# Performance work log

Measured on AMD Instinct MI355X. Metric: run time of the kernel, lower is better.

The kernel has to match this reference:

```python
import jax, jax.numpy as jnp
import numpy as np

B, V, C = 256, 50, 40
VOCAB, D, H, NH, T = 10000, 256, 256, 8, 1000


def setup_inputs():
    key = jax.random.key(0)
    ks = jax.random.split(key, 24)
    f = lambda k, shape, s=0.05: jax.random.normal(k, shape, jnp.float32) * s
    # nn.Embedding(vocab_size+1, d_model, padding_idx=-1): last row is the padding row (zeros)
    emb = f(ks[0], (VOCAB + 1, D), 0.1).at[VOCAB].set(0.0)
    return dict(
        input_seqs=jax.random.randint(ks[1], (B, V, C), 0, VOCAB),
        seq_time_step=jax.random.uniform(ks[2], (B, V), jnp.float32, 0.0, 365.0),
        diffusion_time_t=jax.random.randint(ks[3], (B,), 0, T),
        normal_noise=jax.random.normal(ks[4], (B, V, D), jnp.float32),
        predicted_noise=jax.random.normal(ks[5], (B, V, D), jnp.float32),
        emb=emb,
        betas=jnp.asarray(np.linspace(1e-4, 0.02, T, dtype=np.float32)),
        tl_w=f(ks[6], (64, 1), 0.5), tl_b=f(ks[7], (64,), 0.1),
        tu_w=f(ks[8], (D, 64)), tu_b=f(ks[9], (D,), 0.01),
        in_proj_w=f(ks[10], (3 * D, D)), in_proj_b=f(ks[11], (3 * D,), 0.01),
        out_proj_w=f(ks[12], (D, D)), out_proj_b=f(ks[13], (D,), 0.01),
        w_ih=f(ks[14], (4 * H, D)), w_hh=f(ks[15], (4 * H, H)),
        b_ih=f(ks[16], (4 * H,), 0.01), b_hh=f(ks[17], (4 * H,), 0.01),
        c1_w=f(ks[18], (4 * H, H)), c1_b=f(ks[19], (4 * H,), 0.01),
        c2_w=f(ks[20], (4 * H, 4 * H)), c2_b=f(ks[21], (4 * H,), 0.01),
        co_w=f(ks[22], (2, 4 * H)), co_b=f(ks[23], (2,), 0.01),
    )


def _mha(q, kv, wi, bi, wo, bo):
    # torch MultiheadAttention on 2-D inputs -> unbatched; 'sequence length' = batch dim B
    hd = D // NH
    qp = (q @ wi[:D].T + bi[:D]).reshape(-1, NH, hd)
    kp = (kv @ wi[D:2 * D].T + bi[D:2 * D]).reshape(-1, NH, hd)
    vp = (kv @ wi[2 * D:].T + bi[2 * D:]).reshape(-1, NH, hd)
    s = jnp.einsum('qhd,khd->hqk', qp, kp) * (hd ** -0.5)
    o = jnp.einsum('hqk,khd->qhd', jax.nn.softmax(s, -1), vp).reshape(-1, D)
    return o @ wo.T + bo


def _lstm_final(seq, w_ih, w_hh, b_ih, b_hh):
    # unbatched nn.LSTM over the batch axis (length B). The original's try-branch always
    # raises (seq_h squeezed to 1-D), so the zero-init except-branch runs every visit.
    xg = seq @ w_ih.T + (b_ih + b_hh)  # [B, 4H]
    def step(carry, x):
        h, c = carry
        i, fg, g, o = jnp.split(x + h @ w_hh.T, 4)
        c = jax.nn.sigmoid(fg) * c + jax.nn.sigmoid(i) * jnp.tanh(g)
        h = jax.nn.sigmoid(o) * jnp.tanh(c)
        return (h, c), None
    z = jnp.zeros((H,), seq.dtype)
    (h, _), _ = jax.lax.scan(step, (z, z), xg)
    return h  # [H]


def _classify(h, w1, b1, w2, b2, wo, bo):
    h = jax.nn.relu(h @ w1.T + b1)
    h = jax.nn.relu(h @ w2.T + b2)
    return jax.nn.softmax(h @ wo.T + bo, -1)


def reference(input_seqs, seq_time_step, diffusion_time_t, normal_noise, predicted_noise,
              emb, betas, tl_w, tl_b, tu_w, tu_b, in_proj_w, in_proj_b, out_proj_w,
              out_proj_b, w_ih, w_hh, b_ih, b_hh, c1_w, c1_b, c2_w, c2_b, co_w, co_b):
    tt = seq_time_step[..., None] / 180.0
    tenc = (1.0 - jnp.tanh((tt @ tl_w.T + tl_b) ** 2)) @ tu_w.T + tu_b  # [B,V,D]
    ve = jax.nn.relu(emb[input_seqs]).sum(-2) + tenc                     # [B,V,D]
    alpha = jnp.cumprod(1.0 - betas)[diffusion_time_t][:, None, None]
    ven = ve * jnp.sqrt(alpha) + normal_noise * jnp.sqrt(1.0 - alpha)
    gen1 = ve + (ven - predicted_noise)
    # gen2 recurrence: row i = MHA(row i-1, gen1[:,i], gen1[:,i]); row -1 is the
    # vocab_size-filled initial tensor (valid negative index, try never fails).
    def att_step(prev, kv):
        out = _mha(prev, kv, in_proj_w, in_proj_b, out_proj_w, out_proj_b)
        return out, out
    _, gen2 = jax.lax.scan(att_step, jnp.full((B, D), float(VOCAB), ve.dtype),
                           gen1.transpose(1, 0, 2))                    # [V,B,D]
    lstm = lambda s: _lstm_final(s, w_ih, w_hh, b_ih, b_hh)
    hv = jax.vmap(lstm)(ve.transpose(1, 0, 2))  # [V,H]
    hg = jax.vmap(lstm)(gen2)                   # [V,H]
    res = jnp.broadcast_to(_classify(hv, c1_w, c1_b, c2_w, c2_b, co_w, co_b)[None], (B, V, 2))
    resg = jnp.broadcast_to(_classify(hg, c1_w, c1_b, c2_w, c2_b, co_w, co_b)[None], (B, V, 2))
    return (res, resg, res[:, -1], resg[:, -1], normal_noise, predicted_noise)
```

## Files before the change

kernel.cpp:

```cpp
#include <hip/hip_runtime.h>

#define BB 256
#define VV 50
#define CC 40
#define DD 256
#define HH 256
#define NHH 8
#define TT 1000

typedef unsigned short u16;
typedef unsigned int u32;
typedef _Float16 h2v __attribute__((ext_vector_type(2)));

__device__ __forceinline__ float blf(u16 x){ union{u32 u; float f;} z; z.u=(u32)x<<16; return z.f; }
__device__ __forceinline__ float ld(const void* p, long i, int f){
  if(f) return ((const float*)p)[i];
  return blf(((const u16*)p)[i]);
}
__device__ __forceinline__ u32 packh2(float a, float b){
  union { h2v h; u32 u; } z;
  z.h = h2v{(_Float16)a, (_Float16)b};
  return z.u;
}
__device__ __forceinline__ float fdot2(u32 a, u32 b, float c){
#if __has_builtin(__builtin_amdgcn_fdot2)
  union { u32 u; h2v h; } x, y; x.u=a; y.u=b;
  return __builtin_amdgcn_fdot2(x.h, y.h, c, false);
#else
  union { u32 u; _Float16 h[2]; } x, y; x.u=a; y.u=b;
  return c + (float)x.h[0]*(float)y.h[0] + (float)x.h[1]*(float)y.h[1];
#endif
}
__device__ __forceinline__ float sigm(float x){ return 1.f/(1.f+__expf(-x)); }
__device__ __forceinline__ float tanh_fast(float x){ return 1.f - 2.f/(__expf(2.f*x)+1.f); }


__device__ __forceinline__ void prep_body(const void* betas, int f, int t,
                                          float* sqa, float* s1a, float* sp){
  float om[4]; float p = 1.f;
  #pragma unroll
  for(int k=0;k<4;k++){ int i=t*4+k; float be=(i<TT)?ld(betas,i,f):0.f; om[k]=1.f-be; p*=om[k]; }
  sp[t]=p; __syncthreads();
  for(int off=1; off<256; off<<=1){
    float x = (t>=off) ? sp[t-off]*sp[t] : sp[t];
    __syncthreads(); sp[t]=x; __syncthreads();
  }
  float c = (t>0)? sp[t-1] : 1.f;
  #pragma unroll
  for(int k=0;k<4;k++){
    c *= om[k]; int i=t*4+k;
    if(i<TT){ sqa[i]=sqrtf(c); s1a[i]=sqrtf(fmaxf(1.f-c,0.f)); }
  }
}

__device__ __forceinline__ void packQO_body(const void* src, u32* dst, long elemoff,
                                            int f, int lb, int t){
  int i = lb*256 + t;
  if(i >= 32768) return;
  int c2 = i >> 8, j = i & 255;
  float a = ld(src, elemoff + (long)j*256 + 2*c2,     f);
  float b = ld(src, elemoff + (long)j*256 + 2*c2 + 1, f);
  dst[(c2>>2)*1024 + j*4 + (c2&3)] = packh2(a,b);
}

__device__ __forceinline__ void packH_body(const void* src, u32* dst, int N, int K,
                                           int f, int lb, int t){
  int i = lb*256 + t;
  int tot = N*(K>>1);
  if(i >= tot) return;
  int c2 = i / N, j = i - c2*N;
  float a = ld(src, (long)j*K + 2*c2,     f);
  float b = ld(src, (long)j*K + 2*c2 + 1, f);
  dst[(c2>>2)*(N*4) + j*4 + (c2&3)] = packh2(a,b);
}

__device__ __forceinline__ void packT_body(const void* src, float* dst, int N, int K,
                                           int f, int lb, int t){
  int i = lb*256 + t;
  int tot = N*(K>>2);
  if(i>=tot) return;
  int d4 = i / N, j = i - d4*N;
  long o = (long)j*K + (d4<<2);
  float4 r; r.x=ld(src,o,f); r.y=ld(src,o+1,f); r.z=ld(src,o+2,f); r.w=ld(src,o+3,f);
  ((float4*)dst)[i] = r;
}

__device__ __forceinline__ void packW2_body(const void* src, u32* whhR, u32* wclQ,
                                            int f, int lb, int t){
  int i = lb*256 + t;
  if(i >= 131072) return;
  int row = i >> 7, cp = i & 127;
  float a = ld(src, (long)row*256 + 2*cp,     f);
  float b = ld(src, (long)row*256 + 2*cp + 1, f);
  u32 v = packh2(a,b);
  int q = cp >> 5, pp = cp & 31;
  int rb = row & 127, m = row >> 7;
  int j = q*128 + rb;
  if(pp < 24){
    int idx = m*24 + pp;
    whhR[(idx>>2)*2048 + j*4 + (idx&3)] = v;
  } else {
    int h = (pp-24) >> 2, e = (pp-24) & 3;
    wclQ[((m*2+h)*512 + j)*4 + e] = v;
  }
}

__global__ void k_mega(const void* betas, const void* ipw, const void* opw,
    const void* wih, const void* whh, const void* c1w, const void* c2w, const void* tu_w,
    int* flag, float* sqa, float* s1a,
    u32* wkP, u32* wvP, u32* wqp, u32* wop, u32* wihP,
    u32* whhR, u32* wclQ, u32* c1p, u32* c2p, float* tu4){
  __shared__ float sp[256];
  int f = (((const u32*)betas)[0] == 0x38D1B717u) ? 1 : 0;
  int g = blockIdx.x, t = threadIdx.x;
  if(g == 0){
    if(t == 0) flag[0] = f;
    prep_body(betas, f, t, sqa, s1a, sp);
  }
  else if(g < 129)  packQO_body(ipw, wkP, 65536L,  f, g-1,   t);
  else if(g < 257)  packQO_body(ipw, wvP, 131072L, f, g-129, t);
  else if(g < 385)  packQO_body(ipw, wqp, 0L,      f, g-257, t);
  else if(g < 513)  packQO_body(opw, wop, 0L,      f, g-385, t);
  else if(g < 1025) packH_body(wih, wihP, 1024, 256,  f, g-513,  t);
  else if(g < 1537) packW2_body(whh, whhR, wclQ,      f, g-1025, t);
  else if(g < 2049) packH_body(c1w, c1p, 1024, 256,   f, g-1537, t);
  else if(g < 4097) packH_body(c2w, c2p, 1024, 1024,  f, g-2049, t);
  else              packT_body(tu_w, tu4, 256, 64,    f, g-4097, t);
}

__global__ void k_ve_gen1(const int* seqs, const void* sts, const int* dt,
    const void* nn, const void* pn, const void* emb, const void* tl_w, const void* tl_b,
    const float* tu4, const void* tu_b, const float* sqa, const float* s1a, const int* fl,
    float* ve, float* gen1, float* out){
  int bv = blockIdx.x; int b = bv / VV;
  int t = threadIdx.x;
  int f = fl[0];
  __shared__ float4 f4[16];
  __shared__ int idx[CC];
  float tt = ld(sts,bv,f) * (1.f/180.f);
  if(t<64){ float x = tt*ld(tl_w,t,f) + ld(tl_b,t,f); ((float*)f4)[t] = 1.f - tanhf(x*x); }
  if(t<CC) idx[t] = seqs[bv*CC+t];
  __syncthreads();
  float acc = ld(tu_b,t,f);
  const float4* tu = (const float4*)tu4;
  #pragma unroll
  for(int d4=0; d4<16; d4++){
    float4 w = tu[d4*DD + t];
    float4 fv = f4[d4];
    acc += fv.x*w.x+fv.y*w.y+fv.z*w.z+fv.w*w.w;
  }
  float s=0.f;
  for(int c=0;c<CC;c++){ float e = ld(emb,(long)idx[c]*DD + t,f); s += fmaxf(e,0.f); }
  float vev = s + acc;
  ve[bv*DD+t] = vev;
  int tb = dt[b];
  float sa=sqa[tb], s1=s1a[tb];
  long gi = (long)bv*DD + t;
  float nnv = ld(nn,gi,f);
  float pnv = ld(pn,gi,f);
  gen1[gi] = vev*(1.f+sa) + nnv*s1 - pnv;
  const int n = BB*VV*DD;
  out[52224 + gi]     = nnv;
  out[52224 + n + gi] = pnv;
}

__global__ void k_kvproj(const float* gen1, const u32* wkP, const u32* wvP,
                         const void* bi, const int* fl, u32* kpHq, u32* vp){
  int g = blockIdx.x; int v = g>>4; int b0 = (g&15)<<4;
  int t = threadIdx.x;
  int f = fl[0];
  __shared__ __align__(16) u32 xp[16][128];
  for(int r=0;r<16;r++){
    float xv = gen1[((b0+r)*VV + v)*DD + t];
    float xb = __shfl_xor(xv, 1, 64);
    if((t&1)==0) xp[r][t>>1] = packh2(xv, xb);
  }
  __syncthreads();
  float ak[16], av[16];
  float bk = ld(bi,DD+t,f), bvv = ld(bi,2*DD+t,f);
  #pragma unroll
  for(int r=0;r<16;r++){ ak[r]=bk; av[r]=bvv; }
  const uint4* wk4 = (const uint4*)wkP;
  const uint4* wv4 = (const uint4*)wvP;
  for(int c8=0;c8<32;c8++){
    uint4 kk = wk4[c8*256+t], vv = wv4[c8*256+t];
    #pragma unroll
    for(int r=0;r<16;r++){
      uint4 xx = ((const uint4*)xp[r])[c8];
      ak[r] = fdot2(xx.x, kk.x, ak[r]); ak[r] = fdot2(xx.y, kk.y, ak[r]);
      ak[r] = fdot2(xx.z, kk.z, ak[r]); ak[r] = fdot2(xx.w, kk.w, ak[r]);
      av[r] = fdot2(xx.x, vv.x, av[r]); av[r] = fdot2(xx.y, vv.y, av[r]);
      av[r] = fdot2(xx.z, vv.z, av[r]); av[r] = fdot2(xx.w, vv.w, av[r]);
    }
  }
  #pragma unroll
  for(int r=0;r<16;r++){
    float a2 = __shfl_xor(ak[r], 1, 64);
    if((t&1)==0)
      kpHq[(size_t)v*32768 + (t>>3)*1024 + (size_t)(b0+r)*4 + ((t>>1)&3)] = packh2(ak[r], a2);
  }
  #pragma unroll
  for(int i2=0;i2<8;i2++){
    int k2 = (b0>>1) + i2;
    vp[(size_t)v*32768 + (k2>>2)*1024 + t*4 + (k2&3)] = packh2(av[2*i2], av[2*i2+1]);
  }
}

__global__ __launch_bounds__(256) void k_mha_all(const u32* kpHq, const u32* vp,
    const u32* wqp, const u32* wop, const void* ipb, const void* opb, const int* fl,
    float* gen2){
  int i = blockIdx.x, t = threadIdx.x;
  int f = fl[0];
  __shared__ __align__(16) u32 kls[32768];
  __shared__ __align__(16) u32 xp[128];
  __shared__ __align__(16) u32 qpp[128];
  __shared__ float s[NHH][257];
  __shared__ __align__(16) u32 sp[NHH][128];
  __shared__ __align__(16) u32 op[128];
  __shared__ float mh[NHH], rs[NHH];
  float bq = ld(ipb, t, f);
  float bo = ld(opb, t, f);
  if(t < 128) xp[t] = packh2(10000.f, 10000.f);
  __syncthreads();
  const uint4* xp4 = (const uint4*)xp;
  const uint4* op4 = (const uint4*)op;
  const uint4* wq4p = (const uint4*)wqp;
  const uint4* wo4p = (const uint4*)wop;
  const uint4* kls4 = (const uint4*)kls;
  const uint4* qp4  = (const uint4*)qpp;
  int hg = t>>5, ln = t&31;
  for(int v=0; v<VV; v++){
    {
      const u32* kg = kpHq + (size_t)v*32768;
#if __has_builtin(__builtin_amdgcn_global_load_lds)
      #pragma unroll
      for(int j=0;j<32;j++){
        __builtin_amdgcn_global_load_lds(
          (const __attribute__((address_space(1))) u32*)(kg + (j*256 + t)*4),
          (__attribute__((address_space(3))) u32*)(kls + (j*256 + t)*4), 16, 0, 0);
      }
#else
      const uint4* kg4 = (const uint4*)kg;
      uint4* kl4 = (uint4*)kls;
      #pragma unroll 8
      for(int j=0;j<32;j++) kl4[j*256+t] = kg4[j*256+t];
#endif
    }
    {
      float acc = bq;
      #pragma unroll 8
      for(int c8=0;c8<32;c8++){
        uint4 xx = xp4[c8];
        uint4 ww = wq4p[c8*256 + t];
        acc = fdot2(xx.x, ww.x, acc); acc = fdot2(xx.y, ww.y, acc);
        acc = fdot2(xx.z, ww.z, acc); acc = fdot2(xx.w, ww.w, acc);
      }
      float aq2 = __shfl_xor(acc, 1, 64);
      if((t&1)==0) qpp[t>>1] = packh2(acc, aq2);
    }
    asm volatile("s_waitcnt vmcnt(0)" ::: "memory");
    __syncthreads();
    {
      #pragma unroll
      for(int h=0; h<NHH; h++){
        float acc = 0.f;
        #pragma unroll
        for(int dd=0; dd<4; dd++){
          uint4 kk = kls4[(h*4+dd)*256 + t];
          uint4 qq = qp4[h*4+dd];
          acc = fdot2(qq.x, kk.x, acc); acc = fdot2(qq.y, kk.y, acc);
          acc = fdot2(qq.z, kk.z, acc); acc = fdot2(qq.w, kk.w, acc);
        }
        s[h][t] = acc*0.1767766952966369f;
      }
    }
    __syncthreads();
    float m=-3.0e38f;
    for(int k=ln;k<BB;k+=32) m=fmaxf(m, s[hg][k]);
    for(int off=16;off;off>>=1) m=fmaxf(m, __shfl_down(m,off,32));
    if(ln==0) mh[hg]=m;
    __syncthreads();
    #pragma unroll
    for(int h=0;h<NHH;h++) s[h][t]=__expf(s[h][t]-mh[h]);
    __syncthreads();
    float sm=0.f;
    for(int k=ln;k<BB;k+=32) sm += s[hg][k];
    for(int off=16;off;off>>=1) sm += __shfl_down(sm,off,32);
    if(ln==0) rs[hg]=1.f/sm;
    #pragma unroll
    for(int m2=t; m2<1024; m2+=256){
      int h = m2>>7, k2 = m2&127;
      sp[h][k2] = packh2(s[h][2*k2], s[h][2*k2+1]);
    }
    __syncthreads();
    {
      const uint4* vb = (const uint4*)(vp + (size_t)v*32768);
      const uint4* spv = (const uint4*)sp[hg];
      float acc = 0.f;
      #pragma unroll 8
      for(int k8=0;k8<32;k8++){
        uint4 pv = spv[k8];
        uint4 vv = vb[k8*256 + t];
        acc = fdot2(pv.x, vv.x, acc); acc = fdot2(pv.y, vv.y, acc);
        acc = fdot2(pv.z, vv.z, acc); acc = fdot2(pv.w, vv.w, acc);
      }
      float o = acc * rs[hg];
      float oo = __shfl_xor(o, 1, 64);
      if((t&1)==0) op[t>>1] = packh2(o, oo);
    }
    __syncthreads();
    {
      float acc = bo;
      #pragma unroll 8
      for(int c8=0;c8<32;c8++){
        uint4 xx = op4[c8];
        uint4 ww = wo4p[c8*256 + t];
        acc = fdot2(xx.x, ww.x, acc); acc = fdot2(xx.y, ww.y, acc);
        acc = fdot2(xx.z, ww.z, acc); acc = fdot2(xx.w, ww.w, acc);
      }
      gen2[((size_t)v*BB+i)*DD + t] = acc;
      float ax = __shfl_xor(acc, 1, 64);
      if((t&1)==0) xp[t>>1] = packh2(acc, ax);
    }
    __syncthreads();
  }
}

__global__ __launch_bounds__(256, 2) void k_xg(const float* inp, int is_ve, const u32* wihP,
                     const void* b_ih, const void* b_hh, const int* fl, u16* xg){
  int g = blockIdx.x; int v=g>>4; int b0=(g&15)<<4;
  int t = threadIdx.x;
  int f = fl[0];
  __shared__ __align__(16) u32 xp[16][128];
  for(int r=0;r<16;r++){
    int b = b0+r;
    const float* src = is_ve ? (inp + (b*VV+v)*DD) : (inp + (v*BB+b)*DD);
    float xv = src[t];
    float xb = __shfl_xor(xv, 1, 64);
    if((t&1)==0) xp[r][t>>1] = packh2(xv, xb);
  }
  __syncthreads();
  float acc[4][16];
  #pragma unroll
  for(int js=0;js<4;js++){
    float bsum = ld(b_ih,js*256+t,f) + ld(b_hh,js*256+t,f);
    #pragma unroll
    for(int r=0;r<16;r++) acc[js][r]=bsum;
  }
  const uint4* wp4 = (const uint4*)wihP;
  for(int c8=0; c8<32; c8++){
    uint4 w[4];
    #pragma unroll
    for(int js=0;js<4;js++) w[js] = wp4[c8*1024 + js*256 + t];
    #pragma unroll
    for(int r=0;r<16;r++){
      uint4 xx = ((const uint4*)xp[r])[c8];
      #pragma unroll
      for(int js=0;js<4;js++){
        acc[js][r] = fdot2(xx.x, w[js].x, acc[js][r]);
        acc[js][r] = fdot2(xx.y, w[js].y, acc[js][r]);
        acc[js][r] = fdot2(xx.z, w[js].z, acc[js][r]);
        acc[js][r] = fdot2(xx.w, w[js].w, acc[js][r]);
      }
    }
  }
  for(int r=0;r<16;r++)
    #pragma unroll
    for(int js=0;js<4;js++){
      union { _Float16 h; u16 u; } z;
      z.h = (_Float16)acc[js][r];
      xg[(size_t)(v*BB + b0 + r)*1024 + js*256 + t] = z.u;
    }
}

__global__ __attribute__((amdgpu_flat_work_group_size(512,512)))
__attribute__((amdgpu_waves_per_eu(2,2)))
void k_lstm3(const u16* xgA, const u16* xgB,
    const u32* whhR, const u32* wclQ, float* hfin){
  int b = blockIdx.x, j = threadIdx.x;
  int q = j >> 7, rb = j & 127;
  const u16* xgv = (b < VV) ? (xgA + (size_t)b*BB*1024) : (xgB + (size_t)(b-VV)*BB*1024);
  __shared__ __align__(16) u32 wcl[32768];
  __shared__ __align__(16) float pacc[4][1024];
  __shared__ __align__(16) u32 hp[128];
  u32 w[192];
  { const uint4* wr4 = (const uint4*)whhR;
    #pragma unroll
    for(int i4=0;i4<48;i4++){
      uint4 v = wr4[i4*512 + j];
      w[i4*4+0]=v.x; w[i4*4+1]=v.y; w[i4*4+2]=v.z; w[i4*4+3]=v.w;
    } }
  {
    const uint4* src = (const uint4*)wclQ;
    uint4* dst = (uint4*)wcl;
    #pragma unroll
    for(int i=0;i<16;i++) dst[i*512 + j] = src[i*512 + j];
  }
  if(j < 128) hp[j] = 0u;
  float c0 = 0.f, h_t = 0.f;
  __syncthreads();
  const uint4* hp4 = (const uint4*)hp;
  const uint4* wcl4 = (const uint4*)wcl;
  for(int s=0; s<BB; s++){
    asm volatile("" ::: "memory");
    u16 nx0=0,nx1=0,nx2=0,nx3=0;
    if(j < 256){
      nx0 = xgv[s*1024 +       j];
      nx1 = xgv[s*1024 + 256 + j];
      nx2 = xgv[s*1024 + 512 + j];
      nx3 = xgv[s*1024 + 768 + j];
    }
    float acc[8];
    #pragma unroll
    for(int m=0;m<8;m++) acc[m]=0.f;
    #pragma unroll
    for(int i=0;i<6;i++){
      uint4 hh = hp4[q*8 + i];
      #pragma unroll
      for(int m=0;m<8;m++){
        acc[m] = fdot2(hh.x, w[m*24 + i*4+0], acc[m]);
        acc[m] = fdot2(hh.y, w[m*24 + i*4+1], acc[m]);
        acc[m] = fdot2(hh.z, w[m*24 + i*4+2], acc[m]);
        acc[m] = fdot2(hh.w, w[m*24 + i*4+3], acc[m]);
      }
    }
    #pragma unroll
    for(int h=0;h<2;h++){
      uint4 hh = hp4[q*8 + 6 + h];
      #pragma unroll
      for(int m=0;m<8;m++){
        uint4 s4 = wcl4[(m*2+h)*512 + j];
        acc[m] = fdot2(hh.x, s4.x, acc[m]);
        acc[m] = fdot2(hh.y, s4.y, acc[m]);
        acc[m] = fdot2(hh.z, s4.z, acc[m]);
        acc[m] = fdot2(hh.w, s4.w, acc[m]);
      }
    }
    #pragma unroll
    for(int m=0;m<8;m++) pacc[q][m*128 + rb] = acc[m];
    __syncthreads();
    if(j < 256){
      float a0 = pacc[0][      j] + pacc[1][      j] + pacc[2][      j] + pacc[3][      j];
      float a1 = pacc[0][256 + j] + pacc[1][256 + j] + pacc[2][256 + j] + pacc[3][256 + j];
      float a2 = pacc[0][512 + j] + pacc[1][512 + j] + pacc[2][512 + j] + pacc[3][512 + j];
      float a3 = pacc[0][768 + j] + pacc[1][768 + j] + pacc[2][768 + j] + pacc[3][768 + j];
      float ai = a0 + (float)(*(const _Float16*)&nx0);
      float af = a1 + (float)(*(const _Float16*)&nx1);
      float ag = a2 + (float)(*(const _Float16*)&nx2);
      float ao = a3 + (float)(*(const _Float16*)&nx3);
      float ig = sigm(ai), fg = sigm(af), og = sigm(ao);
      float gg = tanh_fast(ag);
      c0 = fg*c0 + ig*gg;
      h_t = og*tanh_fast(c0);
      float ho = __shfl_xor(h_t, 1, 64);
      if((j&1)==0) hp[j>>1] = packh2(h_t, ho);
    }
    __syncthreads();
  }
  if(j < 256) hfin[b*HH + j] = h_t;
}

__global__ void k_cls(const float* hfin, const u32* c1p, const void* c1b,
                      const u32* c2p, const void* c2b, const void* cow, const void* cob,
                      const int* fl, float* cls){
  int blk = blockIdx.x;
  int t = threadIdx.x;
  int f = fl[0];
  __shared__ __align__(16) u32 hp1[128];
  __shared__ __align__(16) u32 h2p[512];
  __shared__ float h24[1024];
  __shared__ float red0[4], red1[4];
  {
    float hv = hfin[blk*HH + t];
    float hb = __shfl_xor(hv, 1, 64);
    if((t&1)==0) hp1[t>>1] = packh2(hv, hb);
  }
  __syncthreads();
  const uint4* hp14 = (const uint4*)hp1;
  const uint4* c1p4 = (const uint4*)c1p;
  {
    float a[4];
    #pragma unroll
    for(int js=0;js<4;js++) a[js]=ld(c1b,js*256+t,f);
    #pragma unroll 8
    for(int c8=0;c8<32;c8++){
      uint4 hh = hp14[c8];
      #pragma unroll
      for(int js=0;js<4;js++){
        uint4 ww = c1p4[c8*1024 + js*256+t];
        a[js] = fdot2(hh.x, ww.x, a[js]); a[js] = fdot2(hh.y, ww.y, a[js]);
        a[js] = fdot2(hh.z, ww.z, a[js]); a[js] = fdot2(hh.w, ww.w, a[js]);
      }
    }
    #pragma unroll
    for(int js=0;js<4;js++){
      float v = fmaxf(a[js],0.f);
      float vb = __shfl_xor(v, 1, 64);
      if((t&1)==0) h2p[(js*256+t)>>1] = packh2(v, vb);
    }
  }
  __syncthreads();
  const uint4* h2p4 = (const uint4*)h2p;
  const uint4* c2p4 = (const uint4*)c2p;
  {
    float a[4];
    #pragma unroll
    for(int js=0;js<4;js++) a[js]=ld(c2b,js*256+t,f);
    #pragma unroll 8
    for(int c8=0;c8<128;c8++){
      uint4 hh = h2p4[c8];
      #pragma unroll
      for(int js=0;js<4;js++){
        uint4 ww = c2p4[c8*1024 + js*256+t];
        a[js] = fdot2(hh.x, ww.x, a[js]); a[js] = fdot2(hh.y, ww.y, a[js]);
        a[js] = fdot2(hh.z, ww.z, a[js]); a[js] = fdot2(hh.w, ww.w, a[js]);
      }
    }
    #pragma unroll
    for(int js=0;js<4;js++) h24[js*256+t] = fmaxf(a[js],0.f);
  }
  __syncthreads();
  float p0=0.f,p1=0.f;
  #pragma unroll
  for(int js=0;js<4;js++){
    int j=js*256+t;
    float hv=h24[j];
    p0 += hv*ld(cow,j,f);
    p1 += hv*ld(cow,1024+j,f);
  }
  for(int off=32;off;off>>=1){ p0+=__shfl_down(p0,off,64); p1+=__shfl_down(p1,off,64); }
  if((t&63)==0){ red0[t>>6]=p0; red1[t>>6]=p1; }
  __syncthreads();
  if(t==0){
    float l0 = ld(cob,0,f) + red0[0]+red0[1]+red0[2]+red0[3];
    float l1 = ld(cob,1,f) + red1[0]+red1[1]+red1[2]+red1[3];
    float mm = fmaxf(l0,l1);
    float e0=__expf(l0-mm), e1=__expf(l1-mm);
    float inv = 1.f/(e0+e1);
    cls[blk*2] = e0*inv; cls[blk*2+1] = e1*inv;
  }
}

__global__ void k_out(const float* cls, float* out){
  int i = blockIdx.x*256 + threadIdx.x;
  if(i < BB*VV*2){
    int v = (i>>1) % VV, k = i&1;
    out[i] = cls[v*2+k];
    out[BB*VV*2 + i] = cls[(VV+v)*2+k];
  }
  if(i < BB*2){
    int k=i&1;
    out[2*BB*VV*2 + i]        = cls[(VV-1)*2+k];
    out[2*BB*VV*2 + BB*2 + i] = cls[(2*VV-1)*2+k];
  }
}

extern "C" void kernel_launch(void* const* d_in, const int* in_sizes, int n_in,
                              void* d_out, int out_size, void* d_ws, size_t ws_size,
                              hipStream_t stream){
  const int* seqs = (const int*)d_in[0];
  const void* sts  = d_in[1];
  const int* dt   = (const int*)d_in[2];
  const void* nn   = d_in[3];
  const void* pn   = d_in[4];
  const void* emb  = d_in[5];
  const void* betas= d_in[6];
  const void* tl_w = d_in[7];
  const void* tl_b = d_in[8];
  const void* tu_w = d_in[9];
  const void* tu_b = d_in[10];
  const void* ipw  = d_in[11];
  const void* ipb  = d_in[12];
  const void* opw  = d_in[13];
  const void* opb  = d_in[14];
  const void* wih  = d_in[15];
  const void* whh  = d_in[16];
  const void* bih  = d_in[17];
  const void* bhh  = d_in[18];
  const void* c1w  = d_in[19];
  const void* c1b  = d_in[20];
  const void* c2w  = d_in[21];
  const void* c2b  = d_in[22];
  const void* cow  = d_in[23];
  const void* cob  = d_in[24];

  char* base = (char*)d_ws;
  u32*   wkP  = (u32*)(base + 0);
  u32*   wvP  = (u32*)(base + 131072);
  u32*   wqp  = (u32*)(base + 524288);
  u32*   wop  = (u32*)(base + 655360);
  u32*   wihP = (u32*)(base + 786432);
  u32*   whhR = (u32*)(base + 1835008);
  u32*   wclQ = (u32*)(base + 2228224);
  u32*   c1p  = (u32*)(base + 2359296);
  u32*   c2p  = (u32*)(base + 3407872);
  float* tu4  = (float*)(base + 7602176);
  float* sqa  = (float*)(base + 7667712);
  float* s1a  = (float*)(base + 7671808);
  float* hfin = (float*)(base + 7675904);
  float* cls  = (float*)(base + 7778304);
  int*   flag = (int*)(base + 7779328);
  float* ve   = (float*)(base + 7783424);
  float* g12  = (float*)(base + 20890624);
  char*  arena= base + 33997824;
  u32*   kpHq = (u32*)(arena);
  u32*   vp   = (u32*)(arena + 13107200);
  u16*   xgA  = (u16*)(arena);
  u16*   xgB  = (u16*)(arena + 26214400);
  float* out  = (float*)d_out;

  k_mega<<<4113,256,0,stream>>>(betas, ipw, opw, wih, whh, c1w, c2w, tu_w,
      flag, sqa, s1a, wkP, wvP, wqp, wop, wihP, whhR, wclQ, c1p, c2p, tu4);

  k_ve_gen1<<<BB*VV,256,0,stream>>>(seqs,sts,dt,nn,pn,emb,tl_w,tl_b,tu4,tu_b,sqa,s1a,flag,ve,g12,out);

  k_kvproj<<<VV*16,256,0,stream>>>(g12, wkP, wvP, ipb, flag, kpHq, vp);
  k_mha_all<<<BB,256,0,stream>>>(kpHq, vp, wqp, wop, ipb, opb, flag, g12);

  k_xg<<<VV*16,256,0,stream>>>(ve,  1, wihP, bih, bhh, flag, xgA);
  k_xg<<<VV*16,256,0,stream>>>(g12, 0, wihP, bih, bhh, flag, xgB);
  k_lstm3<<<100,512,0,stream>>>(xgA, xgB, whhR, wclQ, hfin);

  k_cls<<<2*VV,256,0,stream>>>(hfin, c1p, c1b, c2p, c2b, cow, cob, flag, cls);
  k_out<<<100,256,0,stream>>>(cls, out);
}
```

Before: 1.531 ms.

## Merge KV projection with ve LSTM input projection; fold output broadcast into classifier

Fuses the K/V projection and the ve-side LSTM input-gate GEMM into one 1600-block launch. The ve GEMM is independent of the attention recurrence, so this fills the GPU better and cuts a launch. It also removes the separate output-broadcast kernel by having each classifier block write its softmax result directly to all batch rows. The arena is relaid out so xgA no longer aliases the K/V buffers that k_mha_all still reads. The fused kernel's launch bounds now apply to the kvproj path, which may change its register allocation.

New measurement: 1.507 ms. About the same (-1.5%).

```diff
diff --git a/kernel.cpp b/kernel.cpp
--- a/kernel.cpp
+++ b/kernel.cpp
@@ -164,12 +164,11 @@
   out[52224 + n + gi] = pnv;
 }
 
-__global__ void k_kvproj(const float* gen1, const u32* wkP, const u32* wvP,
-                         const void* bi, const int* fl, u32* kpHq, u32* vp){
-  int g = blockIdx.x; int v = g>>4; int b0 = (g&15)<<4;
-  int t = threadIdx.x;
-  int f = fl[0];
-  __shared__ __align__(16) u32 xp[16][128];
+
+__device__ __forceinline__ void kvproj_body(const float* gen1, const u32* wkP,
+    const u32* wvP, const void* bi, int f, int g, int t, u32* kpHq, u32* vp,
+    u32 (*xp)[128]){
+  int v = g>>4; int b0 = (g&15)<<4;
   for(int r=0;r<16;r++){
     float xv = gen1[((b0+r)*VV + v)*DD + t];
     float xb = __shfl_xor(xv, 1, 64);
@@ -204,6 +203,68 @@
     int k2 = (b0>>1) + i2;
     vp[(size_t)v*32768 + (k2>>2)*1024 + t*4 + (k2&3)] = packh2(av[2*i2], av[2*i2+1]);
   }
+}
+
+__device__ __forceinline__ void xg_body(const float* inp, int is_ve, const u32* wihP,
+    const void* b_ih, const void* b_hh, int f, int g, int t, u16* xg,
+    u32 (*xp)[128]){
+  int v=g>>4; int b0=(g&15)<<4;
+  for(int r=0;r<16;r++){
+    int b = b0+r;
+    const float* src = is_ve ? (inp + (b*VV+v)*DD) : (inp + (v*BB+b)*DD);
+    float xv = src[t];
+    float xb = __shfl_xor(xv, 1, 64);
+    if((t&1)==0) xp[r][t>>1] = packh2(xv, xb);
+  }
+  __syncthreads();
+  float acc[4][16];
+  #pragma unroll
+  for(int js=0;js<4;js++){
+    float bsum = ld(b_ih,js*256+t,f) + ld(b_hh,js*256+t,f);
+    #pragma unroll
+    for(int r=0;r<16;r++) acc[js][r]=bsum;
+  }
+  const uint4* wp4 = (const uint4*)wihP;
+  for(int c8=0; c8<32; c8++){
+    uint4 w[4];
+    #pragma unroll
+    for(int js=0;js<4;js++) w[js] = wp4[c8*1024 + js*256 + t];
+    #pragma unroll
+    for(int r=0;r<16;r++){
+      uint4 xx = ((const uint4*)xp[r])[c8];
+      #pragma unroll
+      for(int js=0;js<4;js++){
+        acc[js][r] = fdot2(xx.x, w[js].x, acc[js][r]);
+        acc[js][r] = fdot2(xx.y, w[js].y, acc[js][r]);
+        acc[js][r] = fdot2(xx.z, w[js].z, acc[js][r]);
+        acc[js][r] = fdot2(xx.w, w[js].w, acc[js][r]);
+      }
+    }
+  }
+  for(int r=0;r<16;r++)
+    #pragma unroll
+    for(int js=0;js<4;js++){
+      union { _Float16 h; u16 u; } z;
+      z.h = (_Float16)acc[js][r];
+      xg[(size_t)(v*BB + b0 + r)*1024 + js*256 + t] = z.u;
+    }
+}
+
+__global__ __launch_bounds__(256, 2) void k_kvxg(const float* gen1, const float* ve,
+    const u32* wkP, const u32* wvP, const void* bi,
+    const u32* wihP, const void* b_ih, const void* b_hh,
+    const int* fl, u32* kpHq, u32* vp, u16* xgA){
+  __shared__ __align__(16) u32 xp[16][128];
+  int g = blockIdx.x, t = threadIdx.x;
+  int f = fl[0];
+  if(g < 800) kvproj_body(gen1, wkP, wvP, bi, f, g, t, kpHq, vp, xp);
+  else        xg_body(ve, 1, wihP, b_ih, b_hh, f, g-800, t, xgA, xp);
+}
+
+__global__ __launch_bounds__(256, 2) void k_xg(const float* inp, const u32* wihP,
+                     const void* b_ih, const void* b_hh, const int* fl, u16* xg){
+  __shared__ __align__(16) u32 xp[16][128];
+  xg_body(inp, 0, wihP, b_ih, b_hh, fl[0], blockIdx.x, threadIdx.x, xg, xp);
 }
 
 __global__ __launch_bounds__(256) void k_mha_all(const u32* kpHq, const u32* vp,
@@ -326,53 +387,6 @@
   }
 }
 
-__global__ __launch_bounds__(256, 2) void k_xg(const float* inp, int is_ve, const u32* wihP,
-                     const void* b_ih, const void* b_hh, const int* fl, u16* xg){
-  int g = blockIdx.x; int v=g>>4; int b0=(g&15)<<4;
-  int t = threadIdx.x;
-  int f = fl[0];
-  __shared__ __align__(16) u32 xp[16][128];
-  for(int r=0;r<16;r++){
-    int b = b0+r;
-    const float* src = is_ve ? (inp + (b*VV+v)*DD) : (inp + (v*BB+b)*DD);
-    float xv = src[t];
-    float xb = __shfl_xor(xv, 1, 64);
-    if((t&1)==0) xp[r][t>>1] = packh2(xv, xb);
-  }
-  __syncthreads();
-  float acc[4][16];
-  #pragma unroll
-  for(int js=0;js<4;js++){
-    float bsum = ld(b_ih,js*256+t,f) + ld(b_hh,js*256+t,f);
-    #pragma unroll
-    for(int r=0;r<16;r++) acc[js][r]=bsum;
-  }
-  const uint4* wp4 = (const uint4*)wihP;
-  for(int c8=0; c8<32; c8++){
-    uint4 w[4];
-    #pragma unroll
-    for(int js=0;js<4;js++) w[js] = wp4[c8*1024 + js*256 + t];
-    #pragma unroll
-    for(int r=0;r<16;r++){
-      uint4 xx = ((const uint4*)xp[r])[c8];
-      #pragma unroll
-      for(int js=0;js<4;js++){
-        acc[js][r] = fdot2(xx.x, w[js].x, acc[js][r]);
-        acc[js][r] = fdot2(xx.y, w[js].y, acc[js][r]);
-        acc[js][r] = fdot2(xx.z, w[js].z, acc[js][r]);
-        acc[js][r] = fdot2(xx.w, w[js].w, acc[js][r]);
-      }
-    }
-  }
-  for(int r=0;r<16;r++)
-    #pragma unroll
-    for(int js=0;js<4;js++){
-      union { _Float16 h; u16 u; } z;
-      z.h = (_Float16)acc[js][r];
-      xg[(size_t)(v*BB + b0 + r)*1024 + js*256 + t] = z.u;
-    }
-}
-
 __global__ __attribute__((amdgpu_flat_work_group_size(512,512)))
 __attribute__((amdgpu_waves_per_eu(2,2)))
 void k_lstm3(const u16* xgA, const u16* xgB,
@@ -462,7 +476,7 @@
 
 __global__ void k_cls(const float* hfin, const u32* c1p, const void* c1b,
                       const u32* c2p, const void* c2b, const void* cow, const void* cob,
-                      const int* fl, float* cls){
+                      const int* fl, float* out){
   int blk = blockIdx.x;
   int t = threadIdx.x;
   int f = fl[0];
@@ -470,6 +484,7 @@
   __shared__ __align__(16) u32 h2p[512];
   __shared__ float h24[1024];
   __shared__ float red0[4], red1[4];
+  __shared__ float sc2[2];
   {
     float hv = hfin[blk*HH + t];
     float hb = __shfl_xor(hv, 1, 64);
@@ -537,21 +552,21 @@
     float mm = fmaxf(l0,l1);
     float e0=__expf(l0-mm), e1=__expf(l1-mm);
     float inv = 1.f/(e0+e1);
-    cls[blk*2] = e0*inv; cls[blk*2+1] = e1*inv;
-  }
-}
-
-__global__ void k_out(const float* cls, float* out){
-  int i = blockIdx.x*256 + threadIdx.x;
-  if(i < BB*VV*2){
-    int v = (i>>1) % VV, k = i&1;
-    out[i] = cls[v*2+k];
-    out[BB*VV*2 + i] = cls[(VV+v)*2+k];
-  }
-  if(i < BB*2){
-    int k=i&1;
-    out[2*BB*VV*2 + i]        = cls[(VV-1)*2+k];
-    out[2*BB*VV*2 + BB*2 + i] = cls[(2*VV-1)*2+k];
+    sc2[0] = e0*inv; sc2[1] = e1*inv;
+  }
+  __syncthreads();
+  {
+    float c0v = sc2[0], c1v = sc2[1];
+    int isg = (blk >= VV);
+    int v = isg ? (blk - VV) : blk;
+    long base = (isg ? (long)BB*VV*2 : 0) + (long)t*(VV*2) + v*2;
+    out[base]     = c0v;
+    out[base + 1] = c1v;
+    if(v == VV-1){
+      long tbase = 2L*BB*VV*2 + (isg ? BB*2 : 0) + (long)t*2;
+      out[tbase]     = c0v;
+      out[tbase + 1] = c1v;
+    }
   }
 }
 
@@ -598,15 +613,14 @@
   float* sqa  = (float*)(base + 7667712);
   float* s1a  = (float*)(base + 7671808);
   float* hfin = (float*)(base + 7675904);
-  float* cls  = (float*)(base + 7778304);
   int*   flag = (int*)(base + 7779328);
   float* ve   = (float*)(base + 7783424);
   float* g12  = (float*)(base + 20890624);
   char*  arena= base + 33997824;
   u32*   kpHq = (u32*)(arena);
   u32*   vp   = (u32*)(arena + 13107200);
-  u16*   xgA  = (u16*)(arena);
-  u16*   xgB  = (u16*)(arena + 26214400);
+  u16*   xgA  = (u16*)(arena + 26214400);
+  u16*   xgB  = (u16*)(arena);
   float* out  = (float*)d_out;
 
   k_mega<<<4113,256,0,stream>>>(betas, ipw, opw, wih, whh, c1w, c2w, tu_w,
@@ -614,13 +628,11 @@
 
   k_ve_gen1<<<BB*VV,256,0,stream>>>(seqs,sts,dt,nn,pn,emb,tl_w,tl_b,tu4,tu_b,sqa,s1a,flag,ve,g12,out);
 
-  k_kvproj<<<VV*16,256,0,stream>>>(g12, wkP, wvP, ipb, flag, kpHq, vp);
+  k_kvxg<<<1600,256,0,stream>>>(g12, ve, wkP, wvP, ipb, wihP, bih, bhh, flag, kpHq, vp, xgA);
   k_mha_all<<<BB,256,0,stream>>>(kpHq, vp, wqp, wop, ipb, opb, flag, g12);
 
-  k_xg<<<VV*16,256,0,stream>>>(ve,  1, wihP, bih, bhh, flag, xgA);
-  k_xg<<<VV*16,256,0,stream>>>(g12, 0, wihP, bih, bhh, flag, xgB);
+  k_xg<<<VV*16,256,0,stream>>>(g12, wihP, bih, bhh, flag, xgB);
   k_lstm3<<<100,512,0,stream>>>(xgA, xgB, whhR, wclQ, hfin);
 
-  k_cls<<<2*VV,256,0,stream>>>(hfin, c1p, c1b, c2p, c2b, cow, cob, flag, cls);
-  k_out<<<100,256,0,stream>>>(cls, out);
-}
+  k_cls<<<2*VV,256,0,stream>>>(hfin, c1p, c1b, c2p, c2b, cow, cob, flag, out);
+}
```
